# Kernel optimization log

Measured on AMD Instinct MI355X. Metric: run time of the kernel, lower is better.

The kernel has to match this reference:

```python
import jax, jax.numpy as jnp
import numpy as np

NUM_USER = 20000
NUM_ITEM = 40000
N_NODES = NUM_USER + NUM_ITEM
DIM = 64
V_DIM = 2048
T_DIM = 768
N_EDGES = 1_000_000
K_USER = 40
K_ITEM = 10
N_LAYERS = 2


def setup_inputs() -> dict:
    key = jax.random.key(0)
    ks = iter(jax.random.split(key, 32))

    def xavier(shape):
        s = (2.0 / (shape[0] + shape[-1])) ** 0.5
        return jax.random.normal(next(ks), shape, jnp.float32) * s

    # bipartite user-item interactions, doubled (undirected), as in DRAGON.__init__
    u = jax.random.randint(next(ks), (N_EDGES,), 0, NUM_USER)
    it = jax.random.randint(next(ks), (N_EDGES,), NUM_USER, N_NODES)
    edge_index = jnp.stack([jnp.concatenate([u, it]), jnp.concatenate([it, u])])

    v_feat = jax.random.normal(next(ks), (NUM_ITEM, V_DIM), jnp.float32)
    t_feat = jax.random.normal(next(ks), (NUM_ITEM, T_DIM), jnp.float32)

    # KNN item-item adjacency (top-10 per row) with symmetric-normalized values,
    # mirroring get_knn_adj_mat/compute_normalized_laplacian
    rows = jnp.repeat(jnp.arange(NUM_ITEM), K_ITEM)
    cols = jax.random.randint(next(ks), (NUM_ITEM * K_ITEM,), 0, NUM_ITEM)
    mm_indices = jnp.stack([rows, cols])
    row_sum = jax.ops.segment_sum(jnp.ones(NUM_ITEM * K_ITEM, jnp.float32), rows,
                                  num_segments=NUM_ITEM) + 1e-7
    rinv = row_sum ** -0.5
    mm_values = rinv[rows] * rinv[cols]

    user_graph = jax.random.randint(next(ks), (NUM_USER, K_USER), 0, NUM_USER)
    user_weight_matrix = jax.nn.softmax(
        jax.random.normal(next(ks), (NUM_USER, K_USER), jnp.float32), axis=1)
    weight_u = jax.nn.softmax(
        jax.random.normal(next(ks), (NUM_USER, 2, 1), jnp.float32), axis=1)

    return {
        'edge_index': edge_index,
        'v_feat': v_feat, 't_feat': t_feat,
        'v_pref': xavier((NUM_USER, DIM)), 't_pref': xavier((NUM_USER, DIM)),
        'v_mlp1_w': xavier((V_DIM, 4 * DIM)), 'v_mlp1_b': jnp.zeros(4 * DIM, jnp.float32),
        'v_mlp2_w': xavier((4 * DIM, DIM)), 'v_mlp2_b': jnp.zeros(DIM, jnp.float32),
        't_mlp1_w': xavier((T_DIM, 4 * DIM)), 't_mlp1_b': jnp.zeros(4 * DIM, jnp.float32),
        't_mlp2_w': xavier((4 * DIM, DIM)), 't_mlp2_b': jnp.zeros(DIM, jnp.float32),
        'v_conv_w': xavier((DIM, DIM)), 'v_conv_b': jnp.zeros(DIM, jnp.float32),
        't_conv_w': xavier((DIM, DIM)), 't_conv_b': jnp.zeros(DIM, jnp.float32),
        'weight_u': weight_u,
        'user_graph': user_graph,
        'user_weight_matrix': user_weight_matrix,
        'mm_indices': mm_indices,
        'mm_values': mm_values,
    }


def _l2n(x):
    n = jnp.linalg.norm(x, axis=-1, keepdims=True)
    return x / jnp.maximum(n, 1e-12)


def reference(edge_index, v_feat, t_feat, v_pref, t_pref,
              v_mlp1_w, v_mlp1_b, v_mlp2_w, v_mlp2_b,
              t_mlp1_w, t_mlp1_b, t_mlp2_w, t_mlp2_b,
              v_conv_w, v_conv_b, t_conv_w, t_conv_b,
              weight_u, user_graph, user_weight_matrix,
              mm_indices, mm_values):
    seg = jax.ops.segment_sum
    # GCNConv normalization with self-loops (shared by both branches)
    sl = jnp.arange(N_NODES)
    src = jnp.concatenate([edge_index[0], sl])
    dst = jnp.concatenate([edge_index[1], sl])
    deg = seg(jnp.ones_like(dst, dtype=jnp.float32), dst, num_segments=N_NODES)
    dinv = deg ** -0.5
    norm = (dinv[src] * dinv[dst])[:, None]

    def conv(x, w, b):  # out[dst] += norm * (x @ w)[src], then bias
        return seg(norm * (x @ w)[src], dst, num_segments=N_NODES) + b

    def branch(feat, pref, w1, b1, w2, b2, cw, cb):
        temp = jax.nn.leaky_relu(feat @ w1 + b1) @ w2 + b2  # [I, D]
        x = _l2n(jnp.concatenate([pref, temp], axis=0))      # [N, D]
        h = conv(x, cw, cb)
        h1 = conv(h, cw, cb)
        return x + h + h1

    v_rep = branch(v_feat, v_pref, v_mlp1_w, v_mlp1_b, v_mlp2_w, v_mlp2_b, v_conv_w, v_conv_b)
    t_rep = branch(t_feat, t_pref, t_mlp1_w, t_mlp1_b, t_mlp2_w, t_mlp2_b, t_conv_w, t_conv_b)

    representation = jnp.concatenate([v_rep, t_rep], axis=1)  # [N, 2D]
    wu = weight_u[:, :, 0]  # [U, 2]
    user_rep = jnp.concatenate([wu[:, 0:1] * v_rep[:NUM_USER],
                                wu[:, 1:2] * t_rep[:NUM_USER]], axis=1)  # [U, 2D]
    item_rep = representation[NUM_USER:]  # [I, 2D]

    # User_Graph_sample: weighted sum over sampled user neighborhoods
    h_u = jnp.einsum('uk,ukd->ud', user_weight_matrix, user_rep[user_graph])
    user_rep = user_rep + h_u

    # n_layers of sparse Laplacian propagation over KNN item-item graph
    row, col = mm_indices[0], mm_indices[1]
    h_i = item_rep
    for _ in range(N_LAYERS):
        h_i = seg(mm_values[:, None] * h_i[col], row, num_segments=NUM_ITEM)
    item_rep = item_rep + h_i

    return jnp.concatenate([user_rep, item_rep], axis=0)  # [N, 2D]
```

## Files before the change

### kernel.cpp

```cpp
#include <hip/hip_runtime.h>

#define NUSER 20000
#define NITEM 40000
#define NNODE 60000
#define DIM   64
#define NE    1000000
#define KUSER 40
#define KITEM 10

typedef __attribute__((ext_vector_type(8))) short short8v;
typedef __attribute__((ext_vector_type(4))) float floatx4;

__device__ inline short bf16rne(float f) {
    unsigned u = __builtin_bit_cast(unsigned, f);
    unsigned r = (u + 0x7fffu + ((u >> 16) & 1u)) >> 16;
    return (short)r;
}
__device__ inline unsigned cvt_pk_bf16(float lo, float hi) {
    unsigned r;
    asm("v_cvt_pk_bf16_f32 %0, %1, %2" : "=v"(r) : "v"(lo), "v"(hi));
    return r;
}
__device__ inline float bflo(unsigned v) { return __builtin_bit_cast(float, v << 16); }
__device__ inline float bfhi(unsigned v) { return __builtin_bit_cast(float, v & 0xffff0000u); }

__global__ __launch_bounds__(256) void k_count_pair(const int* __restrict__ uu, const int* __restrict__ it,
                                                    int* __restrict__ cnt) {
    int i = blockIdx.x * 256 + threadIdx.x;
    if (i >= NE) return;
    atomicAdd(&cnt[uu[i]], 1);
    atomicAdd(&cnt[it[i]], 1);
}

__global__ __launch_bounds__(256) void k_scanA(const int* __restrict__ v, int* __restrict__ excl,
                                               int* __restrict__ bsum, float* __restrict__ dinv, int n) {
    __shared__ int s[256];
    int t = threadIdx.x, i = blockIdx.x * 256 + t;
    int orig = (i < n) ? v[i] : 0;
    if (i < n) dinv[i] = 1.0f / sqrtf((float)(orig + 1));
    s[t] = orig; __syncthreads();
    #pragma unroll
    for (int off = 1; off < 256; off <<= 1) {
        int u = (t >= off) ? s[t - off] : 0;
        __syncthreads();
        s[t] += u;
        __syncthreads();
    }
    if (i < n) excl[i] = s[t] - orig;
    if (t == 255) bsum[blockIdx.x] = s[255];
}

__global__ __launch_bounds__(256) void k_scanB(int* __restrict__ bsum, int nb) {
    __shared__ int s[256];
    int t = threadIdx.x;
    int orig = (t < nb) ? bsum[t] : 0;
    s[t] = orig; __syncthreads();
    #pragma unroll
    for (int off = 1; off < 256; off <<= 1) {
        int u = (t >= off) ? s[t - off] : 0;
        __syncthreads();
        s[t] += u;
        __syncthreads();
    }
    if (t < nb) bsum[t] = s[t] - orig;
}

__global__ __launch_bounds__(256) void k_scanC(int* __restrict__ excl, const int* __restrict__ bsum,
                                               int* __restrict__ cursor, int n) {
    int i = blockIdx.x * 256 + threadIdx.x;
    if (i < n) {
        int v = excl[i] + bsum[blockIdx.x];
        excl[i] = v;
        cursor[i] = v;
    }
    if (i == 0) excl[n] = 2 * NE;
}

__global__ __launch_bounds__(256) void k_fill_pair(const int* __restrict__ uu, const int* __restrict__ it,
                                                   const float* __restrict__ dinv, int* __restrict__ cursor,
                                                   unsigned* __restrict__ csr_pkd) {
    int i = blockIdx.x * 256 + threadIdx.x;
    if (i >= NE) return;
    int u = uu[i], t = it[i];
    unsigned pku = ((unsigned)(unsigned short)bf16rne(dinv[u]) << 16) | (unsigned)u;
    unsigned pkt = ((unsigned)(unsigned short)bf16rne(dinv[t]) << 16) | (unsigned)t;
    int pos1 = atomicAdd(&cursor[t], 1);
    csr_pkd[pos1] = pku;
    int pos2 = atomicAdd(&cursor[u], 1);
    csr_pkd[pos2] = pkt;
}

__global__ __launch_bounds__(256) void k_transpose_all(const float* __restrict__ W1v, const float* __restrict__ W1t,
                                                       const float* __restrict__ W2v, const float* __restrict__ W2t,
                                                       short* __restrict__ Bv, short* __restrict__ Bt,
                                                       short* __restrict__ B2v, short* __restrict__ B2t) {
    __shared__ float s[16][17];
    int bid = blockIdx.x;
    const float* B; short* D; int K, N, local;
    if (bid < 2048)      { B = W1v; D = Bv;  K = 2048; N = 256; local = bid; }
    else if (bid < 2816) { B = W1t; D = Bt;  K = 768;  N = 256; local = bid - 2048; }
    else if (bid < 2880) { B = W2v; D = B2v; K = 256;  N = 64;  local = bid - 2816; }
    else                 { B = W2t; D = B2t; K = 256;  N = 64;  local = bid - 2880; }
    int ktiles = K >> 4;
    int k0 = (local % ktiles) * 16, n0 = (local / ktiles) * 16;
    int t = threadIdx.x, tx = t & 15, ty = t >> 4;
    s[ty][tx] = B[(size_t)(k0 + ty) * N + n0 + tx];
    __syncthreads();
    int k = k0 + tx, n = n0 + ty;
    D[(size_t)(k >> 5) * (N * 32) + n * 32 + (k & 31)] = bf16rne(s[tx][ty]);
}

__global__ __launch_bounds__(256) void k_prep(const float* __restrict__ Wv, const float* __restrict__ Wt,
                                              const float* __restrict__ bv, const float* __restrict__ bt,
                                              short* __restrict__ Bcat, float* __restrict__ bw, float* __restrict__ bb) {
    __shared__ float Wld[2][64][65];
    __shared__ float W2ld[2][64][65];
    int t = threadIdx.x;
    for (int id = t; id < 8192; id += 256) {
        int z = id >> 12, k = (id >> 6) & 63, n = id & 63;
        Wld[z][k][n] = (z ? Wt : Wv)[k * 64 + n];
    }
    __syncthreads();
    for (int id = t; id < 8192; id += 256) {
        int z = id >> 12, k = (id >> 6) & 63, n = id & 63;
        float a = 0.f;
        #pragma unroll 8
        for (int m = 0; m < 64; m++) a += Wld[z][k][m] * Wld[z][m][n];
        W2ld[z][k][n] = a;
    }
    __syncthreads();
    for (int id = t; id < 32768; id += 256) {
        int k = id >> 7, n = id & 127;
        int kb = k >> 6, kk = k & 63;
        float v = 0.f;
        if (kb == 0)      { if (n < 64)  v = Wld[0][kk][n]; }
        else if (kb == 1) { if (n >= 64) v = Wld[1][kk][n - 64]; }
        else if (kb == 2) { if (n < 64)  v = W2ld[0][kk][n]; }
        else              { if (n >= 64) v = W2ld[1][kk][n - 64]; }
        Bcat[(k >> 5) * 4096 + n * 32 + (k & 31)] = bf16rne(v);
    }
    if (t < 128) {
        int z = t >> 6, n = t & 63;
        const float* b = z ? bt : bv;
        float a = 0.f;
        #pragma unroll 8
        for (int k = 0; k < 64; k++) a += b[k] * Wld[z][k][n];
        bw[t] = a;
        bb[t] = 2.f * b[n];
    }
}

#define AP   40
#define MIDP 264
#define MBLK 128
#define VBLKS ((NITEM + MBLK - 1) / MBLK)
__global__ __launch_bounds__(512, 4) void mlp_merged(const float* __restrict__ Av, const float* __restrict__ At,
                                                  const short* __restrict__ B1v, const short* __restrict__ B1t,
                                                  const float* __restrict__ b1v, const float* __restrict__ b1t,
                                                  const short* __restrict__ B2v, const short* __restrict__ B2t,
                                                  const float* __restrict__ b2v, const float* __restrict__ b2t,
                                                  unsigned* __restrict__ xbf) {
    __shared__ short smem[MBLK * MIDP];
    short* As = smem;
    short* Bs = smem + 2 * MBLK * AP;
    const bool isV = blockIdx.x < VBLKS;
    const float* A    = isV ? Av : At;
    const short* B1t_ = isV ? B1v : B1t;
    const float* b1   = isV ? b1v : b1t;
    const short* B2t_ = isV ? B2v : B2t;
    const float* b2   = isV ? b2v : b2t;
    const int K = isV ? 2048 : 768;
    const int boff = isV ? 0 : 32;
    const int rowBase = (isV ? blockIdx.x : blockIdx.x - VBLKS) * MBLK;

    const int tid = threadIdx.x;
    const int lane = tid & 63, wid = tid >> 6;
    const int wr = wid >> 2, wc = wid & 3;

    const int sar = tid >> 2, sac = (tid & 3) * 8;
    int aclamp = rowBase + sar; if (aclamp > NITEM - 1) aclamp = NITEM - 1;
    const float* aptr = A + (size_t)aclamp * K + sac;

    const int fk = (lane >> 4) * 8;
    const int faoff = (wr * 64 + (lane & 15)) * AP + fk;
    const int fboff = (wc * 64 + (lane & 15)) * AP + fk;

    floatx4 acc[4][4];
    #pragma unroll
    for (int m = 0; m < 4; m++)
        #pragma unroll
        for (int n = 0; n < 4; n++) acc[m][n] = (floatx4)0.f;

    float4 ra0, ra1;
    short8v rb0, rb1;
    const int nk = K >> 5;

    auto ldg = [&](int ks) {
        const float* ap = aptr + ks * 32;
        ra0 = *(const float4*)(ap);
        ra1 = *(const float4*)(ap + 4);
        const short* bsrc = B1t_ + (size_t)ks * 8192 + tid * 16;
        rb0 = *(const short8v*)(bsrc);
        rb1 = *(const short8v*)(bsrc + 8);
    };
    auto stv = [&](int buf) {
        uint4 av;
        av.x = cvt_pk_bf16(ra0.x, ra0.y); av.y = cvt_pk_bf16(ra0.z, ra0.w);
        av.z = cvt_pk_bf16(ra1.x, ra1.y); av.w = cvt_pk_bf16(ra1.z, ra1.w);
        *(uint4*)&As[buf * (MBLK * AP) + sar * AP + sac] = av;
        short* bd = &Bs[buf * (256 * AP) + (tid >> 1) * AP + (tid & 1) * 16];
        *(short8v*)(bd) = rb0;
        *(short8v*)(bd + 8) = rb1;
    };

    ldg(0); stv(0);
    __syncthreads();
    int cur = 0;
    for (int ks = 0; ks < nk; ++ks) {
        if (ks + 1 < nk) ldg(ks + 1);
        short8v a[4], b[4];
        #pragma unroll
        for (int m = 0; m < 4; m++) a[m] = *(const short8v*)&As[cur * (MBLK * AP) + faoff + m * 16 * AP];
        #pragma unroll
        for (int n = 0; n < 4; n++) b[n] = *(const short8v*)&Bs[cur * (256 * AP) + fboff + n * 16 * AP];
        #pragma unroll
        for (int m = 0; m < 4; m++)
            #pragma unroll
            for (int n = 0; n < 4; n++)
                acc[m][n] = __builtin_amdgcn_mfma_f32_16x16x32_bf16(a[m], b[n], acc[m][n], 0, 0, 0);
        if (ks + 1 < nk) stv(cur ^ 1);
        __syncthreads();
        cur ^= 1;
    }

    unsigned* mid32 = (unsigned*)smem;
    float bcol[4];
    #pragma unroll
    for (int n = 0; n < 4; n++) bcol[n] = b1[wc * 64 + n * 16 + (lane & 15)];
    #pragma unroll
    for (int m = 0; m < 4; m++)
        #pragma unroll
        for (int n = 0; n < 4; n++) {
            int col = wc * 64 + n * 16 + (lane & 15);
            #pragma unroll
            for (int q = 0; q < 4; q++) {
                int row = wr * 64 + m * 16 + (lane >> 4) * 4 + q;
                float v = acc[m][n][q] + bcol[n];
                v = v > 0.f ? v : 0.01f * v;
                float pn = __shfl_xor(v, 1, 64);
                if (!(lane & 1)) mid32[row * 132 + (col >> 1)] = cvt_pk_bf16(v, pn);
            }
        }
    __syncthreads();

    const short* mid = smem;
    floatx4 acc2[4];
    #pragma unroll
    for (int n2 = 0; n2 < 4; n2++) acc2[n2] = (floatx4)0.f;
    const int arow = wid * 16 + (lane & 15);
    #pragma unroll
    for (int ks2 = 0; ks2 < 8; ++ks2) {
        short8v af = *(const short8v*)&mid[arow * MIDP + ks2 * 32 + fk];
        const short* bp = B2t_ + ks2 * 2048 + fk;
        short8v bf4[4];
        #pragma unroll
        for (int n2 = 0; n2 < 4; n2++) bf4[n2] = *(const short8v*)(bp + (n2 * 16 + (lane & 15)) * 32);
        #pragma unroll
        for (int n2 = 0; n2 < 4; n2++)
            acc2[n2] = __builtin_amdgcn_mfma_f32_16x16x32_bf16(af, bf4[n2], acc2[n2], 0, 0, 0);
    }

    float b2c[4];
    #pragma unroll
    for (int n2 = 0; n2 < 4; n2++) b2c[n2] = b2[n2 * 16 + (lane & 15)];
    #pragma unroll
    for (int q = 0; q < 4; ++q) {
        float v[4]; float ss = 0.f;
        #pragma unroll
        for (int n2 = 0; n2 < 4; n2++) { v[n2] = acc2[n2][q] + b2c[n2]; ss += v[n2] * v[n2]; }
        ss += __shfl_xor(ss, 1, 64);
        ss += __shfl_xor(ss, 2, 64);
        ss += __shfl_xor(ss, 4, 64);
        ss += __shfl_xor(ss, 8, 64);
        float sc = 1.f / fmaxf(sqrtf(ss), 1e-12f);
        int lr = wid * 16 + (lane >> 4) * 4 + q;
        int grow = NUSER + rowBase + lr;
        bool ok = (rowBase + lr) < NITEM;
        #pragma unroll
        for (int n2 = 0; n2 < 4; n2++) {
            float xn = v[n2] * sc;
            float pn = __shfl_xor(xn, 1, 64);
            if (ok && !(lane & 1))
                xbf[(size_t)grow * 64 + boff + n2 * 8 + ((lane & 15) >> 1)] = cvt_pk_bf16(xn, pn);
        }
    }
}

__global__ __launch_bounds__(256) void k_l2n_pref(const float* __restrict__ prefv, const float* __restrict__ preft,
                                                  unsigned* __restrict__ xbf) {
    int row = blockIdx.x * 4 + (threadIdx.x >> 6);
    int lane = threadIdx.x & 63;
    if (row >= NUSER) return;
    const float* p = blockIdx.y ? preft : prefv;
    float v = p[(size_t)row * 64 + lane];
    float ss = v * v;
    #pragma unroll
    for (int off = 32; off >= 1; off >>= 1) ss += __shfl_xor(ss, off, 64);
    float xn = v / fmaxf(sqrtf(ss), 1e-12f);
    float pn = __shfl_xor(xn, 1, 64);
    if (!(lane & 1))
        xbf[(size_t)row * 64 + (blockIdx.y ? 32 : 0) + (lane >> 1)] = cvt_pk_bf16(xn, pn);
}

__global__ __launch_bounds__(256) void k_gather_p(const int* __restrict__ rowptr, const unsigned* __restrict__ csr_pkd,
                                                  const float* __restrict__ dinv, const unsigned* __restrict__ in_bf,
                                                  unsigned* __restrict__ out_bf, float* __restrict__ s_out) {
    int row = blockIdx.x * 4 + (threadIdx.x >> 6);
    int lane = threadIdx.x & 63;
    if (row >= NNODE) return;
    int p0 = rowptr[row], p1 = rowptr[row + 1];
    float dr = dinv[row];
    unsigned sv = in_bf[(size_t)row * 64 + lane];
    float ax0 = dr * bflo(sv), ay0 = dr * bfhi(sv);
    float ax1 = 0.f, ay1 = 0.f;
    float wsum = 0.f;
    for (int p = p0; p < p1; p += 64) {
        int c = p1 - p; if (c > 64) c = 64;
        unsigned pk = (lane < c) ? csr_pkd[p + lane] : 0u;
        wsum += bfhi(pk);
        int j = 0;
        for (; j + 4 <= c; j += 4) {
            unsigned e0 = __shfl(pk, j, 64),     e1 = __shfl(pk, j + 1, 64);
            unsigned e2 = __shfl(pk, j + 2, 64), e3 = __shfl(pk, j + 3, 64);
            unsigned v0 = in_bf[(size_t)(e0 & 0xffffu) * 64 + lane];
            unsigned v1 = in_bf[(size_t)(e1 & 0xffffu) * 64 + lane];
            unsigned v2 = in_bf[(size_t)(e2 & 0xffffu) * 64 + lane];
            unsigned v3 = in_bf[(size_t)(e3 & 0xffffu) * 64 + lane];
            float w0 = bfhi(e0), w1 = bfhi(e1), w2 = bfhi(e2), w3 = bfhi(e3);
            ax0 += w0 * bflo(v0); ay0 += w0 * bfhi(v0);
            ax1 += w1 * bflo(v1); ay1 += w1 * bfhi(v1);
            ax0 += w2 * bflo(v2); ay0 += w2 * bfhi(v2);
            ax1 += w3 * bflo(v3); ay1 += w3 * bfhi(v3);
        }
        for (; j < c; ++j) {
            unsigned e = __shfl(pk, j, 64);
            unsigned v = in_bf[(size_t)(e & 0xffffu) * 64 + lane];
            float w = bfhi(e);
            ax0 += w * bflo(v); ay0 += w * bfhi(v);
        }
    }
    out_bf[(size_t)row * 64 + lane] = cvt_pk_bf16(dr * (ax0 + ax1), dr * (ay0 + ay1));
    #pragma unroll
    for (int o = 32; o >= 1; o >>= 1) wsum += __shfl_xor(wsum, o, 64);
    if (lane == 0) s_out[row] = dr * (dr + wsum);
}

__global__ __launch_bounds__(512) void k_gather2_rep(const int* __restrict__ rowptr, const unsigned* __restrict__ csr_pkd,
                                                     const float* __restrict__ dinv, const unsigned* __restrict__ g1,
                                                     const short* __restrict__ Bcat, const unsigned* __restrict__ x_bf,
                                                     const float* __restrict__ s, const float* __restrict__ bw,
                                                     const float* __restrict__ bb, const float* __restrict__ weight_u,
                                                     float* __restrict__ rep0, unsigned* __restrict__ rep_bf) {
    __shared__ short As[16 * 264];
    const int tid = threadIdx.x, lane = tid & 63, w = tid >> 6;
    const int rowBase = blockIdx.x * 16;

    for (int rr = 0; rr < 2; ++rr) {
        int lrow = w * 2 + rr;
        int row = rowBase + lrow;
        int p0 = rowptr[row], p1 = rowptr[row + 1];
        float dr = dinv[row];
        unsigned sv = g1[(size_t)row * 64 + lane];
        float ax0 = dr * bflo(sv), ay0 = dr * bfhi(sv);
        float ax1 = 0.f, ay1 = 0.f;
        for (int p = p0; p < p1; p += 64) {
            int c = p1 - p; if (c > 64) c = 64;
            unsigned pk = (lane < c) ? csr_pkd[p + lane] : 0u;
            int j = 0;
            for (; j + 4 <= c; j += 4) {
                unsigned e0 = __shfl(pk, j, 64),     e1 = __shfl(pk, j + 1, 64);
                unsigned e2 = __shfl(pk, j + 2, 64), e3 = __shfl(pk, j + 3, 64);
                unsigned v0 = g1[(size_t)(e0 & 0xffffu) * 64 + lane];
                unsigned v1 = g1[(size_t)(e1 & 0xffffu) * 64 + lane];
                unsigned v2 = g1[(size_t)(e2 & 0xffffu) * 64 + lane];
                unsigned v3 = g1[(size_t)(e3 & 0xffffu) * 64 + lane];
                float w0 = bfhi(e0), w1 = bfhi(e1), w2 = bfhi(e2), w3 = bfhi(e3);
                ax0 += w0 * bflo(v0); ay0 += w0 * bfhi(v0);
                ax1 += w1 * bflo(v1); ay1 += w1 * bfhi(v1);
                ax0 += w2 * bflo(v2); ay0 += w2 * bfhi(v2);
                ax1 += w3 * bflo(v3); ay1 += w3 * bfhi(v3);
            }
            for (; j < c; ++j) {
                unsigned e = __shfl(pk, j, 64);
                unsigned v = g1[(size_t)(e & 0xffffu) * 64 + lane];
                float wj = bfhi(e);
                ax0 += wj * bflo(v); ay0 += wj * bfhi(v);
            }
        }
        *(unsigned*)&As[lrow * 264 + 2 * lane] = sv;
        *(unsigned*)&As[lrow * 264 + 128 + 2 * lane] = cvt_pk_bf16(dr * (ax0 + ax1), dr * (ay0 + ay1));
    }
    __syncthreads();

    const int fk = (lane >> 4) * 8;
    floatx4 acc = (floatx4)0.f;
    #pragma unroll
    for (int ks = 0; ks < 8; ++ks) {
        short8v af = *(const short8v*)&As[(lane & 15) * 264 + ks * 32 + fk];
        short8v bf = *(const short8v*)(Bcat + ks * 4096 + (w * 16 + (lane & 15)) * 32 + fk);
        acc = __builtin_amdgcn_mfma_f32_16x16x32_bf16(af, bf, acc, 0, 0, 0);
    }
    const int col = w * 16 + (lane & 15);
    const float bwc = bw[col], bbc = bb[col];
    #pragma unroll
    for (int q = 0; q < 4; ++q) {
        int lrow = (lane >> 4) * 4 + q;
        int row = rowBase + lrow;
        unsigned xw = x_bf[(size_t)row * 64 + (col >> 1)];
        float xval = (col & 1) ? bfhi(xw) : bflo(xw);
        float v = acc[q] + xval + s[row] * bwc + bbc;
        float wu = (row < NUSER) ? weight_u[row * 2 + (col >> 6)] : 1.0f;
        v *= wu;
        rep0[(size_t)row * 128 + col] = v;
        float pn = __shfl_xor(v, 1, 64);
        if (!(lane & 1))
            rep_bf[(size_t)row * 64 + (col >> 1)] = cvt_pk_bf16(v, pn);
    }
}

#define UBLK (NUSER * 64 / 256)
__global__ __launch_bounds__(256) void k_user_item1(const float* __restrict__ rep0, const unsigned* __restrict__ rep_bf,
                                                    const int* __restrict__ ug, const float* __restrict__ uwm,
                                                    const int* __restrict__ mm_col, const float* __restrict__ mm_values,
                                                    float* __restrict__ out, unsigned* __restrict__ tmp_bf) {
    int bid = blockIdx.x;
    if (bid < UBLK) {
        int id = bid * 256 + threadIdx.x;
        int u = id >> 6, lane = id & 63;
        float2 acc = *(const float2*)(rep0 + (size_t)u * 128 + 2 * lane);
        #pragma unroll 4
        for (int k = 0; k < KUSER; k++) {
            int nb = ug[u * KUSER + k];
            float w = uwm[u * KUSER + k];
            unsigned v = rep_bf[(size_t)nb * 64 + lane];
            acc.x += w * bflo(v);
            acc.y += w * bfhi(v);
        }
        *(float2*)(out + (size_t)u * 128 + 2 * lane) = acc;
    } else {
        int id = (bid - UBLK) * 256 + threadIdx.x;
        int r = id >> 6, lane = id & 63;
        float ax = 0.f, ay = 0.f;
        #pragma unroll
        for (int j = 0; j < KITEM; j++) {
            int c = mm_col[r * KITEM + j];
            float w = mm_values[r * KITEM + j];
            unsigned v = rep_bf[(size_t)(NUSER + c) * 64 + lane];
            ax += w * bflo(v);
            ay += w * bfhi(v);
        }
        tmp_bf[(size_t)r * 64 + lane] = cvt_pk_bf16(ax, ay);
    }
}

__global__ __launch_bounds__(256) void k_item2(const float* __restrict__ rep0, const unsigned* __restrict__ tmp_bf,
                                               const int* __restrict__ mm_col, const float* __restrict__ mm_values,
                                               float* __restrict__ out) {
    int id = blockIdx.x * 256 + threadIdx.x;
    int r = id >> 6, lane = id & 63;
    if (r >= NITEM) return;
    float ax = 0.f, ay = 0.f;
    #pragma unroll
    for (int j = 0; j < KITEM; j++) {
        int c = mm_col[r * KITEM + j];
        float w = mm_values[r * KITEM + j];
        unsigned v = tmp_bf[(size_t)c * 64 + lane];
        ax += w * bflo(v);
        ay += w * bfhi(v);
    }
    float2 base = *(const float2*)(rep0 + (size_t)(NUSER + r) * 128 + 2 * lane);
    float2 o;
    o.x = base.x + ax;
    o.y = base.y + ay;
    *(float2*)(out + (size_t)(NUSER + r) * 128 + 2 * lane) = o;
}

extern "C" void kernel_launch(void* const* d_in, const int* in_sizes, int n_in,
                              void* d_out, int out_size, void* d_ws, size_t ws_size,
                              hipStream_t stream) {
    const int*   edge_index = (const int*)d_in[0];
    const float* v_feat   = (const float*)d_in[1];
    const float* t_feat   = (const float*)d_in[2];
    const float* v_pref   = (const float*)d_in[3];
    const float* t_pref   = (const float*)d_in[4];
    const float* v_mlp1_w = (const float*)d_in[5];
    const float* v_mlp1_b = (const float*)d_in[6];
    const float* v_mlp2_w = (const float*)d_in[7];
    const float* v_mlp2_b = (const float*)d_in[8];
    const float* t_mlp1_w = (const float*)d_in[9];
    const float* t_mlp1_b = (const float*)d_in[10];
    const float* t_mlp2_w = (const float*)d_in[11];
    const float* t_mlp2_b = (const float*)d_in[12];
    const float* v_conv_w = (const float*)d_in[13];
    const float* v_conv_b = (const float*)d_in[14];
    const float* t_conv_w = (const float*)d_in[15];
    const float* t_conv_b = (const float*)d_in[16];
    const float* weight_u = (const float*)d_in[17];
    const int*   user_graph = (const int*)d_in[18];
    const float* uwm      = (const float*)d_in[19];
    const int*   mm_indices = (const int*)d_in[20];
    const float* mm_values  = (const float*)d_in[21];
    float* out = (float*)d_out;

    char* wsb = (char*)d_ws;
    size_t off = 0;
    auto alloc = [&](size_t bytes) -> void* {
        void* p = wsb + off;
        off = (off + bytes + 255) & ~(size_t)255;
        return p;
    };
    int*      cnt     = (int*)     alloc(NNODE * 4);
    float*    dinv    = (float*)   alloc(NNODE * 4);
    int*      rowptr  = (int*)     alloc((NNODE + 1) * 4);
    int*      bsum    = (int*)     alloc(256 * 4);
    int*      cursor  = (int*)     alloc(NNODE * 4);
    unsigned* csr_pkd = (unsigned*)alloc((size_t)2 * NE * 4);
    short*    Btw_v   = (short*)   alloc((size_t)2048 * 256 * 2);
    short*    Btw_t   = (short*)   alloc((size_t)768 * 256 * 2);
    short*    W2b_v   = (short*)   alloc((size_t)256 * 64 * 2);
    short*    W2b_t   = (short*)   alloc((size_t)256 * 64 * 2);
    short*    Bcat    = (short*)   alloc((size_t)256 * 128 * 2);
    float*    bw      = (float*)   alloc(128 * 4);
    float*    bb      = (float*)   alloc(128 * 4);
    float*    svec    = (float*)   alloc(NNODE * 4);
    unsigned* x_bf    = (unsigned*)alloc((size_t)NNODE * 64 * 4);
    unsigned* g1      = (unsigned*)alloc((size_t)NNODE * 64 * 4);
    float*    rep0    = (float*)   alloc((size_t)NNODE * 128 * 4);
    unsigned* rep_bf  = (unsigned*)alloc((size_t)NNODE * 64 * 4);
    unsigned* tmp_bf  = (unsigned*)alloc((size_t)NITEM * 64 * 4);
    (void)ws_size; (void)n_in; (void)in_sizes; (void)out_size;

    const int* pairs_u  = edge_index;
    const int* pairs_it = edge_index + NE;
    const int* mm_col = mm_indices + NITEM * KITEM;

    const int NB = (NNODE + 255) / 256;

    hipMemsetAsync(cnt, 0, NNODE * 4, stream);
    k_count_pair<<<(NE + 255) / 256, 256, 0, stream>>>(pairs_u, pairs_it, cnt);
    k_scanA<<<NB, 256, 0, stream>>>(cnt, rowptr, bsum, dinv, NNODE);
    k_scanB<<<1, 256, 0, stream>>>(bsum, NB);
    k_scanC<<<NB, 256, 0, stream>>>(rowptr, bsum, cursor, NNODE);
    k_fill_pair<<<(NE + 255) / 256, 256, 0, stream>>>(pairs_u, pairs_it, dinv, cursor, csr_pkd);

    k_prep<<<1, 256, 0, stream>>>(v_conv_w, t_conv_w, v_conv_b, t_conv_b, Bcat, bw, bb);
    k_transpose_all<<<2944, 256, 0, stream>>>(v_mlp1_w, t_mlp1_w, v_mlp2_w, t_mlp2_w,
                                              Btw_v, Btw_t, W2b_v, W2b_t);

    mlp_merged<<<2 * VBLKS, 512, 0, stream>>>(v_feat, t_feat, Btw_v, Btw_t, v_mlp1_b, t_mlp1_b,
                                              W2b_v, W2b_t, v_mlp2_b, t_mlp2_b, x_bf);
    {
        dim3 g(NUSER / 4, 2);
        k_l2n_pref<<<g, 256, 0, stream>>>(v_pref, t_pref, x_bf);
    }

    k_gather_p<<<(NNODE + 3) / 4, 256, 0, stream>>>(rowptr, csr_pkd, dinv, x_bf, g1, svec);
    k_gather2_rep<<<NNODE / 16, 512, 0, stream>>>(rowptr, csr_pkd, dinv, g1, Bcat, x_bf,
                                                  svec, bw, bb, weight_u, rep0, rep_bf);

    k_user_item1<<<UBLK + NITEM * 64 / 256, 256, 0, stream>>>(rep0, rep_bf, user_graph, uwm,
                                                              mm_col, mm_values, out, tmp_bf);
    k_item2<<<NITEM * 64 / 256, 256, 0, stream>>>(rep0, tmp_bf, mm_col, mm_values, out);
}
```

Before: 567.0 us.

## Merge independent setup kernels into fewer launches via block-range dispatch

Independent stages are combined into shared kernels and chosen by block-index range. Edge counting runs with the weight transposes, the block-sum scan with the conv-weight prep, and the CSR fill with the MLP and the user-pref L2 normalization. This cuts the launch count from 10 to 6 and lets small, latency-bound kernels overlap with heavier ones. In exchange, the fill and l2n blocks now carry the MLP kernel's 512-thread launch bounds and large shared memory, which may lower their occupancy.

```diff
diff --git a/kernel.cpp b/kernel.cpp
--- a/kernel.cpp
+++ b/kernel.cpp
@@ -24,78 +24,24 @@
 __device__ inline float bflo(unsigned v) { return __builtin_bit_cast(float, v << 16); }
 __device__ inline float bfhi(unsigned v) { return __builtin_bit_cast(float, v & 0xffff0000u); }
 
-__global__ __launch_bounds__(256) void k_count_pair(const int* __restrict__ uu, const int* __restrict__ it,
-                                                    int* __restrict__ cnt) {
-    int i = blockIdx.x * 256 + threadIdx.x;
-    if (i >= NE) return;
-    atomicAdd(&cnt[uu[i]], 1);
-    atomicAdd(&cnt[it[i]], 1);
-}
-
-__global__ __launch_bounds__(256) void k_scanA(const int* __restrict__ v, int* __restrict__ excl,
-                                               int* __restrict__ bsum, float* __restrict__ dinv, int n) {
-    __shared__ int s[256];
-    int t = threadIdx.x, i = blockIdx.x * 256 + t;
-    int orig = (i < n) ? v[i] : 0;
-    if (i < n) dinv[i] = 1.0f / sqrtf((float)(orig + 1));
-    s[t] = orig; __syncthreads();
-    #pragma unroll
-    for (int off = 1; off < 256; off <<= 1) {
-        int u = (t >= off) ? s[t - off] : 0;
-        __syncthreads();
-        s[t] += u;
-        __syncthreads();
-    }
-    if (i < n) excl[i] = s[t] - orig;
-    if (t == 255) bsum[blockIdx.x] = s[255];
-}
-
-__global__ __launch_bounds__(256) void k_scanB(int* __restrict__ bsum, int nb) {
-    __shared__ int s[256];
-    int t = threadIdx.x;
-    int orig = (t < nb) ? bsum[t] : 0;
-    s[t] = orig; __syncthreads();
-    #pragma unroll
-    for (int off = 1; off < 256; off <<= 1) {
-        int u = (t >= off) ? s[t - off] : 0;
-        __syncthreads();
-        s[t] += u;
-        __syncthreads();
-    }
-    if (t < nb) bsum[t] = s[t] - orig;
-}
-
-__global__ __launch_bounds__(256) void k_scanC(int* __restrict__ excl, const int* __restrict__ bsum,
-                                               int* __restrict__ cursor, int n) {
-    int i = blockIdx.x * 256 + threadIdx.x;
-    if (i < n) {
-        int v = excl[i] + bsum[blockIdx.x];
-        excl[i] = v;
-        cursor[i] = v;
-    }
-    if (i == 0) excl[n] = 2 * NE;
-}
-
-__global__ __launch_bounds__(256) void k_fill_pair(const int* __restrict__ uu, const int* __restrict__ it,
-                                                   const float* __restrict__ dinv, int* __restrict__ cursor,
-                                                   unsigned* __restrict__ csr_pkd) {
-    int i = blockIdx.x * 256 + threadIdx.x;
-    if (i >= NE) return;
-    int u = uu[i], t = it[i];
-    unsigned pku = ((unsigned)(unsigned short)bf16rne(dinv[u]) << 16) | (unsigned)u;
-    unsigned pkt = ((unsigned)(unsigned short)bf16rne(dinv[t]) << 16) | (unsigned)t;
-    int pos1 = atomicAdd(&cursor[t], 1);
-    csr_pkd[pos1] = pku;
-    int pos2 = atomicAdd(&cursor[u], 1);
-    csr_pkd[pos2] = pkt;
-}
-
-__global__ __launch_bounds__(256) void k_transpose_all(const float* __restrict__ W1v, const float* __restrict__ W1t,
-                                                       const float* __restrict__ W2v, const float* __restrict__ W2t,
-                                                       short* __restrict__ Bv, short* __restrict__ Bt,
-                                                       short* __restrict__ B2v, short* __restrict__ B2t) {
+#define CNTB ((NE + 255) / 256)
+#define TRB  2944
+__global__ __launch_bounds__(256) void k_count_transpose(const int* __restrict__ uu, const int* __restrict__ it,
+                                                         int* __restrict__ cnt,
+                                                         const float* __restrict__ W1v, const float* __restrict__ W1t,
+                                                         const float* __restrict__ W2v, const float* __restrict__ W2t,
+                                                         short* __restrict__ Bv, short* __restrict__ Bt,
+                                                         short* __restrict__ B2v, short* __restrict__ B2t) {
     __shared__ float s[16][17];
     int bid = blockIdx.x;
+    if (bid < CNTB) {
+        int i = bid * 256 + threadIdx.x;
+        if (i >= NE) return;
+        atomicAdd(&cnt[uu[i]], 1);
+        atomicAdd(&cnt[it[i]], 1);
+        return;
+    }
+    bid -= CNTB;
     const float* B; short* D; int K, N, local;
     if (bid < 2048)      { B = W1v; D = Bv;  K = 2048; N = 256; local = bid; }
     else if (bid < 2816) { B = W1t; D = Bt;  K = 768;  N = 256; local = bid - 2048; }
@@ -110,12 +56,46 @@
     D[(size_t)(k >> 5) * (N * 32) + n * 32 + (k & 31)] = bf16rne(s[tx][ty]);
 }
 
-__global__ __launch_bounds__(256) void k_prep(const float* __restrict__ Wv, const float* __restrict__ Wt,
-                                              const float* __restrict__ bv, const float* __restrict__ bt,
-                                              short* __restrict__ Bcat, float* __restrict__ bw, float* __restrict__ bb) {
+__global__ __launch_bounds__(256) void k_scanA(const int* __restrict__ v, int* __restrict__ excl,
+                                               int* __restrict__ bsum, float* __restrict__ dinv, int n) {
+    __shared__ int s[256];
+    int t = threadIdx.x, i = blockIdx.x * 256 + t;
+    int orig = (i < n) ? v[i] : 0;
+    if (i < n) dinv[i] = 1.0f / sqrtf((float)(orig + 1));
+    s[t] = orig; __syncthreads();
+    #pragma unroll
+    for (int off = 1; off < 256; off <<= 1) {
+        int u = (t >= off) ? s[t - off] : 0;
+        __syncthreads();
+        s[t] += u;
+        __syncthreads();
+    }
+    if (i < n) excl[i] = s[t] - orig;
+    if (t == 255) bsum[blockIdx.x] = s[255];
+}
+
+__global__ __launch_bounds__(256) void k_scanB_prep(int* __restrict__ bsum, int nb,
+                                                    const float* __restrict__ Wv, const float* __restrict__ Wt,
+                                                    const float* __restrict__ bv, const float* __restrict__ bt,
+                                                    short* __restrict__ Bcat, float* __restrict__ bw,
+                                                    float* __restrict__ bb) {
     __shared__ float Wld[2][64][65];
     __shared__ float W2ld[2][64][65];
     int t = threadIdx.x;
+    if (blockIdx.x == 0) {
+        int* s = (int*)&Wld[0][0][0];
+        int orig = (t < nb) ? bsum[t] : 0;
+        s[t] = orig; __syncthreads();
+        #pragma unroll
+        for (int off = 1; off < 256; off <<= 1) {
+            int u = (t >= off) ? s[t - off] : 0;
+            __syncthreads();
+            s[t] += u;
+            __syncthreads();
+        }
+        if (t < nb) bsum[t] = s[t] - orig;
+        return;
+    }
     for (int id = t; id < 8192; id += 256) {
         int z = id >> 12, k = (id >> 6) & 63, n = id & 63;
         Wld[z][k][n] = (z ? Wt : Wv)[k * 64 + n];
@@ -150,20 +130,73 @@
     }
 }
 
+__global__ __launch_bounds__(256) void k_scanC(int* __restrict__ excl, const int* __restrict__ bsum,
+                                               int* __restrict__ cursor, int n) {
+    int i = blockIdx.x * 256 + threadIdx.x;
+    if (i < n) {
+        int v = excl[i] + bsum[blockIdx.x];
+        excl[i] = v;
+        cursor[i] = v;
+    }
+    if (i == 0) excl[n] = 2 * NE;
+}
+
 #define AP   40
 #define MIDP 264
 #define MBLK 128
 #define VBLKS ((NITEM + MBLK - 1) / MBLK)
-__global__ __launch_bounds__(512, 4) void mlp_merged(const float* __restrict__ Av, const float* __restrict__ At,
-                                                  const short* __restrict__ B1v, const short* __restrict__ B1t,
-                                                  const float* __restrict__ b1v, const float* __restrict__ b1t,
-                                                  const short* __restrict__ B2v, const short* __restrict__ B2t,
-                                                  const float* __restrict__ b2v, const float* __restrict__ b2t,
-                                                  unsigned* __restrict__ xbf) {
+#define FILLB ((NE + 511) / 512)
+#define MLPB  (2 * VBLKS)
+#define L2NB  (NUSER * 2 / 8)
+__global__ __launch_bounds__(512, 4) void k_fill_mlp_l2n(
+        const int* __restrict__ uu, const int* __restrict__ it, const float* __restrict__ dinv,
+        int* __restrict__ cursor, unsigned* __restrict__ csr_pkd,
+        const float* __restrict__ Av, const float* __restrict__ At,
+        const short* __restrict__ B1v, const short* __restrict__ B1t,
+        const float* __restrict__ b1v, const float* __restrict__ b1t,
+        const short* __restrict__ B2v, const short* __restrict__ B2t,
+        const float* __restrict__ b2v, const float* __restrict__ b2t,
+        const float* __restrict__ prefv, const float* __restrict__ preft,
+        unsigned* __restrict__ xbf) {
     __shared__ short smem[MBLK * MIDP];
+    const int tid = threadIdx.x;
+    int bid = blockIdx.x;
+
+    if (bid < FILLB) {
+        int i = bid * 512 + tid;
+        if (i >= NE) return;
+        int u = uu[i], t = it[i];
+        unsigned pku = ((unsigned)(unsigned short)bf16rne(dinv[u]) << 16) | (unsigned)u;
+        unsigned pkt = ((unsigned)(unsigned short)bf16rne(dinv[t]) << 16) | (unsigned)t;
+        int pos1 = atomicAdd(&cursor[t], 1);
+        csr_pkd[pos1] = pku;
+        int pos2 = atomicAdd(&cursor[u], 1);
+        csr_pkd[pos2] = pkt;
+        return;
+    }
+    bid -= FILLB;
+
+    if (bid >= MLPB) {
+        int lb = bid - MLPB;
+        int lane = tid & 63;
+        int wg = lb * 8 + (tid >> 6);
+        int row = wg >> 1, br = wg & 1;
+        if (row >= NUSER) return;
+        const float* p = br ? preft : prefv;
+        float v = p[(size_t)row * 64 + lane];
+        float ss = v * v;
+        #pragma unroll
+        for (int off = 32; off >= 1; off >>= 1) ss += __shfl_xor(ss, off, 64);
+        float xn = v / fmaxf(sqrtf(ss), 1e-12f);
+        float pn = __shfl_xor(xn, 1, 64);
+        if (!(lane & 1))
+            xbf[(size_t)row * 64 + (br ? 32 : 0) + (lane >> 1)] = cvt_pk_bf16(xn, pn);
+        return;
+    }
+
     short* As = smem;
     short* Bs = smem + 2 * MBLK * AP;
-    const bool isV = blockIdx.x < VBLKS;
+    const bool isV = bid < VBLKS;
     const float* A    = isV ? Av : At;
     const short* B1t_ = isV ? B1v : B1t;
     const float* b1   = isV ? b1v : b1t;
@@ -171,9 +204,8 @@
     const float* b2   = isV ? b2v : b2t;
     const int K = isV ? 2048 : 768;
     const int boff = isV ? 0 : 32;
-    const int rowBase = (isV ? blockIdx.x : blockIdx.x - VBLKS) * MBLK;
-
-    const int tid = threadIdx.x;
+    const int rowBase = (isV ? bid : bid - VBLKS) * MBLK;
+
     const int lane = tid & 63, wid = tid >> 6;
     const int wr = wid >> 2, wc = wid & 3;
 
@@ -294,22 +326,6 @@
                 xbf[(size_t)grow * 64 + boff + n2 * 8 + ((lane & 15) >> 1)] = cvt_pk_bf16(xn, pn);
         }
     }
-}
-
-__global__ __launch_bounds__(256) void k_l2n_pref(const float* __restrict__ prefv, const float* __restrict__ preft,
-                                                  unsigned* __restrict__ xbf) {
-    int row = blockIdx.x * 4 + (threadIdx.x >> 6);
-    int lane = threadIdx.x & 63;
-    if (row >= NUSER) return;
-    const float* p = blockIdx.y ? preft : prefv;
-    float v = p[(size_t)row * 64 + lane];
-    float ss = v * v;
-    #pragma unroll
-    for (int off = 32; off >= 1; off >>= 1) ss += __shfl_xor(ss, off, 64);
-    float xn = v / fmaxf(sqrtf(ss), 1e-12f);
-    float pn = __shfl_xor(xn, 1, 64);
-    if (!(lane & 1))
-        xbf[(size_t)row * 64 + (blockIdx.y ? 32 : 0) + (lane >> 1)] = cvt_pk_bf16(xn, pn);
 }
 
 __global__ __launch_bounds__(256) void k_gather_p(const int* __restrict__ rowptr, const unsigned* __restrict__ csr_pkd,
@@ -547,22 +563,17 @@
     const int NB = (NNODE + 255) / 256;
 
     hipMemsetAsync(cnt, 0, NNODE * 4, stream);
-    k_count_pair<<<(NE + 255) / 256, 256, 0, stream>>>(pairs_u, pairs_it, cnt);
+    k_count_transpose<<<CNTB + TRB, 256, 0, stream>>>(pairs_u, pairs_it, cnt,
+                                                      v_mlp1_w, t_mlp1_w, v_mlp2_w, t_mlp2_w,
+                                                      Btw_v, Btw_t, W2b_v, W2b_t);
     k_scanA<<<NB, 256, 0, stream>>>(cnt, rowptr, bsum, dinv, NNODE);
-    k_scanB<<<1, 256, 0, stream>>>(bsum, NB);
+    k_scanB_prep<<<2, 256, 0, stream>>>(bsum, NB, v_conv_w, t_conv_w, v_conv_b, t_conv_b, Bcat, bw, bb);
     k_scanC<<<NB, 256, 0, stream>>>(rowptr, bsum, cursor, NNODE);
-    k_fill_pair<<<(NE + 255) / 256, 256, 0, stream>>>(pairs_u, pairs_it, dinv, cursor, csr_pkd);
-
-    k_prep<<<1, 256, 0, stream>>>(v_conv_w, t_conv_w, v_conv_b, t_conv_b, Bcat, bw, bb);
-    k_transpose_all<<<2944, 256, 0, stream>>>(v_mlp1_w, t_mlp1_w, v_mlp2_w, t_mlp2_w,
-                                              Btw_v, Btw_t, W2b_v, W2b_t);
-
-    mlp_merged<<<2 * VBLKS, 512, 0, stream>>>(v_feat, t_feat, Btw_v, Btw_t, v_mlp1_b, t_mlp1_b,
-                                              W2b_v, W2b_t, v_mlp2_b, t_mlp2_b, x_bf);
-    {
-        dim3 g(NUSER / 4, 2);
-        k_l2n_pref<<<g, 256, 0, stream>>>(v_pref, t_pref, x_bf);
-    }
+
+    k_fill_mlp_l2n<<<FILLB + MLPB + L2NB, 512, 0, stream>>>(
+        pairs_u, pairs_it, dinv, cursor, csr_pkd,
+        v_feat, t_feat, Btw_v, Btw_t, v_mlp1_b, t_mlp1_b,
+        W2b_v, W2b_t, v_mlp2_b, t_mlp2_b, v_pref, t_pref, x_bf);
 
     k_gather_p<<<(NNODE + 3) / 4, 256, 0, stream>>>(rowptr, csr_pkd, dinv, x_bf, g1, svec);
     k_gather2_rep<<<NNODE / 16, 512, 0, stream>>>(rowptr, csr_pkd, dinv, g1, Bcat, x_bf,
```

Measured after the change: 559.1 us. Within noise of the previous version (-1.4%).
